# Performance work log

Measured on AMD Instinct MI355X. Metric: run time of the kernel, lower is better.

The kernel has to match this reference:

```python
import jax, jax.numpy as jnp
import numpy as np


def _layernorm(x, g, b, eps=1e-5):
    mu = jnp.mean(x, axis=-1, keepdims=True)
    var = jnp.mean(jnp.square(x - mu), axis=-1, keepdims=True)
    return (x - mu) * jax.lax.rsqrt(var + eps) * g + b


def setup_inputs() -> dict:
    key = jax.random.key(0)
    ks = jax.random.split(key, 8)
    dim, ctx_dim, heads, dim_head = 256, 256, 8, 64
    inner = heads * dim_head
    s = 0.02
    return {
        "x": jax.random.normal(ks[0], (4, dim, 64, 64), jnp.float32),
        "y": jax.random.normal(ks[1], (4, 1024, ctx_dim), jnp.float32),
        "ln_x_g": jnp.ones((dim,), jnp.float32),
        "ln_x_b": jnp.zeros((dim,), jnp.float32),
        "ln_y_g": jnp.ones((ctx_dim,), jnp.float32),
        "ln_y_b": jnp.zeros((ctx_dim,), jnp.float32),
        "Wq": jax.random.normal(ks[2], (dim, inner), jnp.float32) * s,
        "Wk": jax.random.normal(ks[3], (ctx_dim, inner), jnp.float32) * s,
        "Wv": jax.random.normal(ks[4], (ctx_dim, inner), jnp.float32) * s,
        "bv": jnp.zeros((inner,), jnp.float32),
        "Wo": jax.random.normal(ks[5], (inner, dim), jnp.float32) * s,
        "bo": jnp.zeros((dim,), jnp.float32),
    }


def reference(x, y, ln_x_g, ln_x_b, ln_y_g, ln_y_b, Wq, Wk, Wv, bv, Wo, bo):
    heads, dim_head = 8, 64
    b, c = x.shape[:2]
    # channel_last=False path: [b, c, H, W] -> [b, n, c]
    xn = x.reshape(b, c, -1).swapaxes(1, 2)
    xn = _layernorm(xn, ln_x_g, ln_x_b)          # note: x is reassigned in torch code
    yn = _layernorm(y, ln_y_g, ln_y_b)
    q = xn @ Wq                                   # [b, n, h*d]
    k = yn @ Wk                                   # [b, m, h*d]
    v = yn @ Wv + bv                              # [b, m, h*d]

    def split_heads(t):
        B, N, _ = t.shape
        return t.reshape(B, N, heads, dim_head).transpose(0, 2, 1, 3)  # [b, h, n, d]

    q, k, v = split_heads(q), split_heads(k), split_heads(v)
    attn = jnp.einsum("bhid,bhjd->bhij", q, k) * (dim_head ** -0.5)
    attn = jax.nn.softmax(attn, axis=-1)
    out = jnp.einsum("bhij,bhjd->bhid", attn, v)  # [b, h, n, d]
    out = out.transpose(0, 2, 1, 3).reshape(b, -1, heads * dim_head)
    out = out @ Wo + bo
    return xn + out  # residual with layernormed x (faithful to source)
```

## Files before the change

### kernel.cpp

```cpp
#include <hip/hip_runtime.h>
#include <hip/hip_bf16.h>
#include <cstddef>

#define BATCH 4
#define CDIM 256
#define HW 4096
#define MCTX 1024
#define CTX 256
#define HEADS 8
#define DHEAD 64
#define INNER 512

typedef __attribute__((ext_vector_type(8))) short bf16x8;
typedef __attribute__((ext_vector_type(4))) float f32x4;

static __device__ __forceinline__ ushort f2bf(float f) {
  __hip_bfloat16 h = __float2bfloat16(f);
  return *reinterpret_cast<ushort*>(&h);
}

__global__ __launch_bounds__(256) void ln_x_kernel(
    const float* __restrict__ x, const float* __restrict__ g,
    const float* __restrict__ bta, float* __restrict__ xn,
    ushort* __restrict__ xnbf) {
  const int blk = blockIdx.x;
  const int bi = blk / (HW / 32);
  const int n0 = (blk % (HW / 32)) * 32;
  __shared__ float xt[32][257];
  __shared__ float smu[32], srs[32];
  const int t = threadIdx.x;
  const int nl = t & 31;
  const int c0 = t >> 5;
  const float* xb = x + (size_t)bi * CDIM * HW;
  #pragma unroll
  for (int c = c0; c < CDIM; c += 8)
    xt[nl][c] = xb[(size_t)c * HW + n0 + nl];
  __syncthreads();
  const int col = t >> 3, j = t & 7;
  float s = 0.f, ss = 0.f;
  #pragma unroll
  for (int c = j; c < CDIM; c += 8) {
    float v = xt[col][c];
    s += v; ss += v * v;
  }
  #pragma unroll
  for (int off = 1; off < 8; off <<= 1) {
    s += __shfl_xor(s, off);
    ss += __shfl_xor(ss, off);
  }
  if (j == 0) {
    float mu = s * (1.f / CDIM);
    smu[col] = mu;
    srs[col] = rsqrtf(ss * (1.f / CDIM) - mu * mu + 1e-5f);
  }
  __syncthreads();
  const float gv = g[t], bvv = bta[t];
  float* xnb = xn + ((size_t)bi * HW + n0) * CDIM;
  ushort* xbb = xnbf + ((size_t)bi * HW + n0) * CDIM;
  #pragma unroll 4
  for (int n = 0; n < 32; ++n) {
    float val = (xt[n][t] - smu[n]) * srs[n] * gv + bvv;
    xnb[(size_t)n * CDIM + t] = val;
    xbb[(size_t)n * CDIM + t] = f2bf(val);
  }
}

__global__ __launch_bounds__(64) void ln_y_kernel(
    const float* __restrict__ y, const float* __restrict__ g,
    const float* __restrict__ bta, ushort* __restrict__ ynbf) {
  const int row = blockIdx.x;
  const int t = threadIdx.x;
  float4 v = ((const float4*)(y + (size_t)row * CTX))[t];
  float s = v.x + v.y + v.z + v.w;
  float ss = v.x * v.x + v.y * v.y + v.z * v.z + v.w * v.w;
  #pragma unroll
  for (int off = 1; off < 64; off <<= 1) {
    s += __shfl_xor(s, off);
    ss += __shfl_xor(ss, off);
  }
  float mu = s * (1.f / CTX);
  float rs = rsqrtf(ss * (1.f / CTX) - mu * mu + 1e-5f);
  float4 gv = ((const float4*)g)[t];
  float4 b4 = ((const float4*)bta)[t];
  ushort4 ob;
  ob.x = f2bf((v.x - mu) * rs * gv.x + b4.x);
  ob.y = f2bf((v.y - mu) * rs * gv.y + b4.y);
  ob.z = f2bf((v.z - mu) * rs * gv.z + b4.z);
  ob.w = f2bf((v.w - mu) * rs * gv.w + b4.w);
  *(ushort4*)(ynbf + (size_t)row * CTX + t * 4) = ob;
}

__global__ __launch_bounds__(256) void wprep_kernel(
    const float* __restrict__ W, ushort* __restrict__ Wt, int K, int N) {
  __shared__ ushort T[64][65];
  const int k0 = blockIdx.y * 64, n0 = blockIdx.x * 64;
  const int t = threadIdx.x;
  #pragma unroll
  for (int rr = 0; rr < 4; ++rr) {
    int row = rr * 16 + (t >> 4);
    int c = (t & 15) * 4;
    float4 wv = *(const float4*)(W + (size_t)(k0 + row) * N + n0 + c);
    T[row][c + 0] = f2bf(wv.x); T[row][c + 1] = f2bf(wv.y);
    T[row][c + 2] = f2bf(wv.z); T[row][c + 3] = f2bf(wv.w);
  }
  __syncthreads();
  #pragma unroll
  for (int rr = 0; rr < 4; ++rr) {
    int nrow = rr * 16 + (t >> 4);
    int kc = (t & 15) * 4;
    ushort4 o;
    o.x = T[kc + 0][nrow]; o.y = T[kc + 1][nrow];
    o.z = T[kc + 2][nrow]; o.w = T[kc + 3][nrow];
    *(ushort4*)(Wt + (size_t)(n0 + nrow) * K + k0 + kc) = o;
  }
}

__global__ __launch_bounds__(256) void vtr_kernel(
    const ushort* __restrict__ v, ushort* __restrict__ vt) {
  const int bh = blockIdx.z, bi = bh >> 3, h = bh & 7;
  const int m0 = blockIdx.x * 64;
  __shared__ ushort T[64][65];
  const int t = threadIdx.x;
  #pragma unroll
  for (int rr = 0; rr < 4; ++rr) {
    int row = rr * 16 + (t >> 4);
    int c = (t & 15) * 4;
    ushort4 vv = *(const ushort4*)(v + (size_t)(bi * MCTX + m0 + row) * INNER + h * DHEAD + c);
    T[row][c + 0] = vv.x; T[row][c + 1] = vv.y;
    T[row][c + 2] = vv.z; T[row][c + 3] = vv.w;
  }
  __syncthreads();
  #pragma unroll
  for (int rr = 0; rr < 4; ++rr) {
    int drow = rr * 16 + (t >> 4);
    int mc = (t & 15) * 4;
    ushort4 o;
    o.x = T[mc + 0][drow]; o.y = T[mc + 1][drow];
    o.z = T[mc + 2][drow]; o.w = T[mc + 3][drow];
    *(ushort4*)(vt + (size_t)(bh * 64 + drow) * MCTX + m0 + mc) = o;
  }
}

template <bool HAS_BIAS, bool F32_RES_OUT>
__global__ __launch_bounds__(256) void mfma_gemm(
    const ushort* __restrict__ A, const ushort* __restrict__ Bt,
    const float* __restrict__ bias, const float* __restrict__ res,
    void* __restrict__ Cout, int M, int N, int K, float scale) {
  __shared__ ushort As[128 * 40];
  __shared__ ushort Bs[128 * 40];
  const int t = threadIdx.x;
  const int l = t & 63, w = t >> 6;
  const int lq = l & 15, lg = l >> 4;
  const int wr = w >> 1, wc = w & 1;
  const int m0 = blockIdx.y * 128, n0 = blockIdx.x * 128;
  f32x4 acc[4][4];
  #pragma unroll
  for (int mt = 0; mt < 4; ++mt)
    #pragma unroll
    for (int nt = 0; nt < 4; ++nt)
      #pragma unroll
      for (int e = 0; e < 4; ++e) acc[mt][nt][e] = 0.f;
  const int r = t >> 2, ch = (t & 3) * 8;
  for (int k0 = 0; k0 < K; k0 += 32) {
    uint4 a0 = *(const uint4*)(A + (size_t)(m0 + r) * K + k0 + ch);
    uint4 a1 = *(const uint4*)(A + (size_t)(m0 + r + 64) * K + k0 + ch);
    uint4 b0 = *(const uint4*)(Bt + (size_t)(n0 + r) * K + k0 + ch);
    uint4 b1 = *(const uint4*)(Bt + (size_t)(n0 + r + 64) * K + k0 + ch);
    __syncthreads();
    *(uint4*)(&As[r * 40 + ch]) = a0;
    *(uint4*)(&As[(r + 64) * 40 + ch]) = a1;
    *(uint4*)(&Bs[r * 40 + ch]) = b0;
    *(uint4*)(&Bs[(r + 64) * 40 + ch]) = b1;
    __syncthreads();
    bf16x8 af[4], bfr[4];
    #pragma unroll
    for (int mt = 0; mt < 4; ++mt)
      af[mt] = *(const bf16x8*)(&As[(wr * 64 + mt * 16 + lq) * 40 + lg * 8]);
    #pragma unroll
    for (int nt = 0; nt < 4; ++nt)
      bfr[nt] = *(const bf16x8*)(&Bs[(wc * 64 + nt * 16 + lq) * 40 + lg * 8]);
    #pragma unroll
    for (int mt = 0; mt < 4; ++mt)
      #pragma unroll
      for (int nt = 0; nt < 4; ++nt)
        acc[mt][nt] = __builtin_amdgcn_mfma_f32_16x16x32_bf16(
            af[mt], bfr[nt], acc[mt][nt], 0, 0, 0);
  }
  #pragma unroll
  for (int nt = 0; nt < 4; ++nt) {
    const int colc = n0 + wc * 64 + nt * 16 + lq;
    const float bcol = HAS_BIAS ? bias[colc] : 0.f;
    #pragma unroll
    for (int mt = 0; mt < 4; ++mt) {
      #pragma unroll
      for (int i = 0; i < 4; ++i) {
        const size_t row = (size_t)(m0 + wr * 64 + mt * 16 + lg * 4 + i);
        float v = acc[mt][nt][i] * scale + bcol;
        if (F32_RES_OUT) {
          ((float*)Cout)[row * N + colc] = v + res[row * N + colc];
        } else {
          ((ushort*)Cout)[row * N + colc] = f2bf(v);
        }
      }
    }
  }
}

__global__ __launch_bounds__(512, 4) void attn_mfma(
    const ushort* __restrict__ q, const ushort* __restrict__ k,
    const ushort* __restrict__ vt, ushort* __restrict__ ao) {
  const int bi = blockIdx.z, h = blockIdx.y;
  const int n0 = blockIdx.x * 256;
  __shared__ ushort Ks[2][64 * 64];
  __shared__ ushort Vs[2][64 * 64];
  __shared__ ushort Ps[8][2][16 * 64];
  const int t = threadIdx.x;
  const int l = t & 63, w = t >> 6;
  const int lq = l & 15, lg = l >> 4;

  bf16x8 bq[2][2];
  #pragma unroll
  for (int g = 0; g < 2; ++g) {
    const size_t qrow = (size_t)(bi * HW + n0 + w * 32 + g * 16 + lq);
    #pragma unroll
    for (int ks = 0; ks < 2; ++ks)
      bq[g][ks] = *(const bf16x8*)(q + qrow * INNER + h * DHEAD + ks * 32 + lg * 8);
  }

  float m_run[2] = {-1e30f, -1e30f}, l_run[2] = {0.f, 0.f};
  f32x4 oacc[2][4];
  #pragma unroll
  for (int g = 0; g < 2; ++g)
    #pragma unroll
    for (int dt = 0; dt < 4; ++dt)
      #pragma unroll
      for (int e = 0; e < 4; ++e) oacc[g][dt][e] = 0.f;

  const int rr = t >> 3, cc = (t & 7) * 8;
  const ushort* kptr = k + (size_t)(bi * MCTX + rr) * INNER + h * DHEAD + cc;
  const ushort* vptr = vt + (size_t)((bi * HEADS + h) * 64 + rr) * MCTX + cc;
  const int sidx = (rr * 64 + cc) ^ ((rr & 7) << 3);

  {
    uint4 k0v = *(const uint4*)(kptr);
    uint4 v0v = *(const uint4*)(vptr);
    *(uint4*)(&Ks[0][sidx]) = k0v;
    *(uint4*)(&Vs[0][sidx]) = v0v;
  }
  __syncthreads();

  #pragma unroll 2
  for (int m0 = 0; m0 < MCTX; m0 += 64) {
    const int buf = (m0 >> 6) & 1;
    const bool more = (m0 + 64) < MCTX;
    uint4 kpre{}, vpre{};
    if (more) {
      kpre = *(const uint4*)(kptr + (size_t)(m0 + 64) * INNER);
      vpre = *(const uint4*)(vptr + (m0 + 64));
    }
    f32x4 sc[2][4];
    #pragma unroll
    for (int g = 0; g < 2; ++g)
      #pragma unroll
      for (int j = 0; j < 4; ++j)
        #pragma unroll
        for (int e = 0; e < 4; ++e) sc[g][j][e] = 0.f;
    __builtin_amdgcn_s_setprio(1);
    #pragma unroll
    for (int j = 0; j < 4; ++j) {
      #pragma unroll
      for (int ks = 0; ks < 2; ++ks) {
        const int krow = j * 16 + lq;
        bf16x8 ak = *(const bf16x8*)(
            &Ks[buf][(krow * 64 + ks * 32 + lg * 8) ^ ((krow & 7) << 3)]);
        sc[0][j] = __builtin_amdgcn_mfma_f32_16x16x32_bf16(ak, bq[0][ks], sc[0][j], 0, 0, 0);
        sc[1][j] = __builtin_amdgcn_mfma_f32_16x16x32_bf16(ak, bq[1][ks], sc[1][j], 0, 0, 0);
      }
    }
    __builtin_amdgcn_s_setprio(0);
    bf16x8 pa[2][2];
    #pragma unroll
    for (int g = 0; g < 2; ++g) {
      float mloc = -1e30f;
      #pragma unroll
      for (int j = 0; j < 4; ++j)
        #pragma unroll
        for (int e = 0; e < 4; ++e) mloc = fmaxf(mloc, sc[g][j][e]);
      mloc = fmaxf(mloc, __shfl_xor(mloc, 16));
      mloc = fmaxf(mloc, __shfl_xor(mloc, 32));
      if (!__all((int)(mloc - m_run[g] <= 8.f))) {
        const float mnew = fmaxf(m_run[g], mloc);
        const float corr = __builtin_amdgcn_exp2f(m_run[g] - mnew);
        l_run[g] *= corr;
        m_run[g] = mnew;
        #pragma unroll
        for (int i = 0; i < 4; ++i) {
          float ci = __shfl(corr, lg * 4 + i);
          #pragma unroll
          for (int dt = 0; dt < 4; ++dt) oacc[g][dt][i] *= ci;
        }
      }
      float psum = 0.f;
      #pragma unroll
      for (int j = 0; j < 4; ++j)
        #pragma unroll
        for (int e = 0; e < 4; ++e) {
          float p = __builtin_amdgcn_exp2f(sc[g][j][e] - m_run[g]);
          sc[g][j][e] = p; psum += p;
        }
      psum += __shfl_xor(psum, 16);
      psum += __shfl_xor(psum, 32);
      l_run[g] += psum;
      #pragma unroll
      for (int j = 0; j < 4; ++j) {
        uint2 pk;
        pk.x = (uint)f2bf(sc[g][j][0]) | ((uint)f2bf(sc[g][j][1]) << 16);
        pk.y = (uint)f2bf(sc[g][j][2]) | ((uint)f2bf(sc[g][j][3]) << 16);
        *(uint2*)(&Ps[w][g][(lq * 64 + j * 16 + lg * 4) ^ ((lq & 7) << 3)]) = pk;
      }
      #pragma unroll
      for (int ks = 0; ks < 2; ++ks)
        pa[g][ks] = *(const bf16x8*)(
            &Ps[w][g][(lq * 64 + ks * 32 + lg * 8) ^ ((lq & 7) << 3)]);
    }
    __builtin_amdgcn_s_setprio(1);
    #pragma unroll
    for (int dt = 0; dt < 4; ++dt) {
      #pragma unroll
      for (int ks = 0; ks < 2; ++ks) {
        const int vrow = dt * 16 + lq;
        bf16x8 vb = *(const bf16x8*)(
            &Vs[buf][(vrow * 64 + ks * 32 + lg * 8) ^ ((vrow & 7) << 3)]);
        oacc[0][dt] = __builtin_amdgcn_mfma_f32_16x16x32_bf16(pa[0][ks], vb, oacc[0][dt], 0, 0, 0);
        oacc[1][dt] = __builtin_amdgcn_mfma_f32_16x16x32_bf16(pa[1][ks], vb, oacc[1][dt], 0, 0, 0);
      }
    }
    __builtin_amdgcn_s_setprio(0);
    if (more) {
      *(uint4*)(&Ks[buf ^ 1][sidx]) = kpre;
      *(uint4*)(&Vs[buf ^ 1][sidx]) = vpre;
    }
    __syncthreads();
  }
  #pragma unroll
  for (int g = 0; g < 2; ++g) {
    const float rl = 1.f / l_run[g];
    #pragma unroll
    for (int i = 0; i < 4; ++i) {
      float li = __shfl(rl, lg * 4 + i);
      const size_t row = (size_t)(bi * HW + n0 + w * 32 + g * 16 + lg * 4 + i);
      #pragma unroll
      for (int dt = 0; dt < 4; ++dt)
        ao[row * INNER + h * DHEAD + dt * 16 + lq] = f2bf(oacc[g][dt][i] * li);
    }
  }
}

extern "C" void kernel_launch(void* const* d_in, const int* in_sizes, int n_in,
                              void* d_out, int out_size, void* d_ws, size_t ws_size,
                              hipStream_t stream) {
  const float* x     = (const float*)d_in[0];
  const float* y     = (const float*)d_in[1];
  const float* ln_xg = (const float*)d_in[2];
  const float* ln_xb = (const float*)d_in[3];
  const float* ln_yg = (const float*)d_in[4];
  const float* ln_yb = (const float*)d_in[5];
  const float* Wq    = (const float*)d_in[6];
  const float* Wk    = (const float*)d_in[7];
  const float* Wv    = (const float*)d_in[8];
  const float* bv    = (const float*)d_in[9];
  const float* Wo    = (const float*)d_in[10];
  const float* bo    = (const float*)d_in[11];
  float* out = (float*)d_out;

  char* p = (char*)d_ws;
  float*  xn   = (float*)p;  p += (size_t)16384 * 256 * 4;
  ushort* xnbf = (ushort*)p; p += (size_t)16384 * 256 * 2;
  ushort* ynbf = (ushort*)p; p += (size_t)4096 * 256 * 2;
  ushort* wtq  = (ushort*)p; p += (size_t)512 * 256 * 2;
  ushort* wtk  = (ushort*)p; p += (size_t)512 * 256 * 2;
  ushort* wtv  = (ushort*)p; p += (size_t)512 * 256 * 2;
  ushort* wto  = (ushort*)p; p += (size_t)256 * 512 * 2;
  ushort* qbf  = (ushort*)p; p += (size_t)16384 * 512 * 2;
  ushort* kbf  = (ushort*)p; p += (size_t)4096 * 512 * 2;
  ushort* vbf  = (ushort*)p; p += (size_t)4096 * 512 * 2;
  ushort* vtb  = (ushort*)p; p += (size_t)4096 * 512 * 2;
  ushort* aobf = (ushort*)p; p += (size_t)16384 * 512 * 2;

  wprep_kernel<<<dim3(8, 4), 256, 0, stream>>>(Wq, wtq, 256, 512);
  wprep_kernel<<<dim3(8, 4), 256, 0, stream>>>(Wk, wtk, 256, 512);
  wprep_kernel<<<dim3(8, 4), 256, 0, stream>>>(Wv, wtv, 256, 512);
  wprep_kernel<<<dim3(4, 8), 256, 0, stream>>>(Wo, wto, 512, 256);
  ln_x_kernel<<<dim3(BATCH * (HW / 32)), 256, 0, stream>>>(x, ln_xg, ln_xb, xn, xnbf);
  ln_y_kernel<<<dim3(BATCH * MCTX), 64, 0, stream>>>(y, ln_yg, ln_yb, ynbf);
  mfma_gemm<false, false><<<dim3(4, 128), 256, 0, stream>>>(
      xnbf, wtq, nullptr, nullptr, qbf, 16384, 512, 256, 0.1803368801111204f);
  mfma_gemm<false, false><<<dim3(4, 32), 256, 0, stream>>>(
      ynbf, wtk, nullptr, nullptr, kbf, 4096, 512, 256, 1.f);
  mfma_gemm<true, false><<<dim3(4, 32), 256, 0, stream>>>(
      ynbf, wtv, bv, nullptr, vbf, 4096, 512, 256, 1.f);
  vtr_kernel<<<dim3(16, 1, 32), 256, 0, stream>>>(vbf, vtb);
  attn_mfma<<<dim3(HW / 256, HEADS, BATCH), 512, 0, stream>>>(qbf, kbf, vtb, aobf);
  mfma_gemm<true, true><<<dim3(2, 128), 256, 0, stream>>>(
      aobf, wto, bo, xn, out, 16384, 256, 512, 1.f);
}
```

Baseline: 129.8 us.

## Shrink attention blocks, single-buffer K/V, batch weight prep and LN-y rows

The attention kernel moves from 512-thread blocks covering 256 query rows to 256-thread blocks covering 128 rows. It drops LDS double buffering and the two-group P staging to cut shared memory per block and raise occupancy (launch bounds 256,6). In exchange, each K/V tile now needs two barriers, one before and one after the LDS store, and the loop unroll hint is removed. Separately, the three QKV weight-prep launches are merged into one z-indexed launch, and the LN-y kernel processes four rows per 256-thread block to cut launch and block overhead.

New measurement: 381.4 us. 194% more time.

```diff
diff --git a/kernel.cpp b/kernel.cpp
--- a/kernel.cpp
+++ b/kernel.cpp
@@ -65,11 +65,11 @@
   }
 }
 
-__global__ __launch_bounds__(64) void ln_y_kernel(
+__global__ __launch_bounds__(256) void ln_y_kernel(
     const float* __restrict__ y, const float* __restrict__ g,
     const float* __restrict__ bta, ushort* __restrict__ ynbf) {
-  const int row = blockIdx.x;
-  const int t = threadIdx.x;
+  const int row = blockIdx.x * 4 + (threadIdx.x >> 6);
+  const int t = threadIdx.x & 63;
   float4 v = ((const float4*)(y + (size_t)row * CTX))[t];
   float s = v.x + v.y + v.z + v.w;
   float ss = v.x * v.x + v.y * v.y + v.z * v.z + v.w * v.w;
@@ -90,7 +90,7 @@
   *(ushort4*)(ynbf + (size_t)row * CTX + t * 4) = ob;
 }
 
-__global__ __launch_bounds__(256) void wprep_kernel(
+static __device__ __forceinline__ void wprep_body(
     const float* __restrict__ W, ushort* __restrict__ Wt, int K, int N) {
   __shared__ ushort T[64][65];
   const int k0 = blockIdx.y * 64, n0 = blockIdx.x * 64;
@@ -113,6 +113,21 @@
     o.z = T[kc + 2][nrow]; o.w = T[kc + 3][nrow];
     *(ushort4*)(Wt + (size_t)(n0 + nrow) * K + k0 + kc) = o;
   }
+}
+
+__global__ __launch_bounds__(256) void wprep3_kernel(
+    const float* __restrict__ W0, const float* __restrict__ W1,
+    const float* __restrict__ W2, ushort* __restrict__ T0,
+    ushort* __restrict__ T1, ushort* __restrict__ T2) {
+  const int z = blockIdx.z;
+  const float* W = (z == 0) ? W0 : (z == 1) ? W1 : W2;
+  ushort* Wt = (z == 0) ? T0 : (z == 1) ? T1 : T2;
+  wprep_body(W, Wt, 256, 512);
+}
+
+__global__ __launch_bounds__(256) void wprep_kernel(
+    const float* __restrict__ W, ushort* __restrict__ Wt, int K, int N) {
+  wprep_body(W, Wt, K, N);
 }
 
 __global__ __launch_bounds__(256) void vtr_kernel(
@@ -206,14 +221,14 @@
   }
 }
 
-__global__ __launch_bounds__(512, 4) void attn_mfma(
+__global__ __launch_bounds__(256, 6) void attn_mfma(
     const ushort* __restrict__ q, const ushort* __restrict__ k,
     const ushort* __restrict__ vt, ushort* __restrict__ ao) {
   const int bi = blockIdx.z, h = blockIdx.y;
-  const int n0 = blockIdx.x * 256;
-  __shared__ ushort Ks[2][64 * 64];
-  __shared__ ushort Vs[2][64 * 64];
-  __shared__ ushort Ps[8][2][16 * 64];
+  const int n0 = blockIdx.x * 128;
+  __shared__ ushort Ks[64 * 64];
+  __shared__ ushort Vs[64 * 64];
+  __shared__ ushort Ps[4][16 * 64];
   const int t = threadIdx.x;
   const int l = t & 63, w = t >> 6;
   const int lq = l & 15, lg = l >> 4;
@@ -236,27 +251,32 @@
       #pragma unroll
       for (int e = 0; e < 4; ++e) oacc[g][dt][e] = 0.f;
 
-  const int rr = t >> 3, cc = (t & 7) * 8;
-  const ushort* kptr = k + (size_t)(bi * MCTX + rr) * INNER + h * DHEAD + cc;
-  const ushort* vptr = vt + (size_t)((bi * HEADS + h) * 64 + rr) * MCTX + cc;
-  const int sidx = (rr * 64 + cc) ^ ((rr & 7) << 3);
+  const int rr0 = t >> 3, cc0 = (t & 7) * 8;
+  const int rr1 = (t + 256) >> 3, cc1 = cc0;
+  const ushort* kbase = k + (size_t)bi * MCTX * INNER + h * DHEAD;
+  const ushort* vbase = vt + (size_t)((bi * HEADS + h) * 64) * MCTX;
+  const int sidx0 = (rr0 * 64 + cc0) ^ ((rr0 & 7) << 3);
+  const int sidx1 = (rr1 * 64 + cc1) ^ ((rr1 & 7) << 3);
 
   {
-    uint4 k0v = *(const uint4*)(kptr);
-    uint4 v0v = *(const uint4*)(vptr);
-    *(uint4*)(&Ks[0][sidx]) = k0v;
-    *(uint4*)(&Vs[0][sidx]) = v0v;
+    uint4 ka = *(const uint4*)(kbase + (size_t)rr0 * INNER + cc0);
+    uint4 kb2 = *(const uint4*)(kbase + (size_t)rr1 * INNER + cc1);
+    uint4 va = *(const uint4*)(vbase + (size_t)rr0 * MCTX + cc0);
+    uint4 vb2 = *(const uint4*)(vbase + (size_t)rr1 * MCTX + cc1);
+    *(uint4*)(&Ks[sidx0]) = ka;  *(uint4*)(&Ks[sidx1]) = kb2;
+    *(uint4*)(&Vs[sidx0]) = va;  *(uint4*)(&Vs[sidx1]) = vb2;
   }
   __syncthreads();
 
-  #pragma unroll 2
   for (int m0 = 0; m0 < MCTX; m0 += 64) {
-    const int buf = (m0 >> 6) & 1;
     const bool more = (m0 + 64) < MCTX;
-    uint4 kpre{}, vpre{};
+    uint4 kp0{}, kp1{}, vp0{}, vp1{};
     if (more) {
-      kpre = *(const uint4*)(kptr + (size_t)(m0 + 64) * INNER);
-      vpre = *(const uint4*)(vptr + (m0 + 64));
+      const int mn = m0 + 64;
+      kp0 = *(const uint4*)(kbase + (size_t)(mn + rr0) * INNER + cc0);
+      kp1 = *(const uint4*)(kbase + (size_t)(mn + rr1) * INNER + cc1);
+      vp0 = *(const uint4*)(vbase + (size_t)rr0 * MCTX + mn + cc0);
+      vp1 = *(const uint4*)(vbase + (size_t)rr1 * MCTX + mn + cc1);
     }
     f32x4 sc[2][4];
     #pragma unroll
@@ -272,7 +292,7 @@
       for (int ks = 0; ks < 2; ++ks) {
         const int krow = j * 16 + lq;
         bf16x8 ak = *(const bf16x8*)(
-            &Ks[buf][(krow * 64 + ks * 32 + lg * 8) ^ ((krow & 7) << 3)]);
+            &Ks[(krow * 64 + ks * 32 + lg * 8) ^ ((krow & 7) << 3)]);
         sc[0][j] = __builtin_amdgcn_mfma_f32_16x16x32_bf16(ak, bq[0][ks], sc[0][j], 0, 0, 0);
         sc[1][j] = __builtin_amdgcn_mfma_f32_16x16x32_bf16(ak, bq[1][ks], sc[1][j], 0, 0, 0);
       }
@@ -316,12 +336,12 @@
         uint2 pk;
         pk.x = (uint)f2bf(sc[g][j][0]) | ((uint)f2bf(sc[g][j][1]) << 16);
         pk.y = (uint)f2bf(sc[g][j][2]) | ((uint)f2bf(sc[g][j][3]) << 16);
-        *(uint2*)(&Ps[w][g][(lq * 64 + j * 16 + lg * 4) ^ ((lq & 7) << 3)]) = pk;
+        *(uint2*)(&Ps[w][(lq * 64 + j * 16 + lg * 4) ^ ((lq & 7) << 3)]) = pk;
       }
       #pragma unroll
       for (int ks = 0; ks < 2; ++ks)
         pa[g][ks] = *(const bf16x8*)(
-            &Ps[w][g][(lq * 64 + ks * 32 + lg * 8) ^ ((lq & 7) << 3)]);
+            &Ps[w][(lq * 64 + ks * 32 + lg * 8) ^ ((lq & 7) << 3)]);
     }
     __builtin_amdgcn_s_setprio(1);
     #pragma unroll
@@ -330,17 +350,18 @@
       for (int ks = 0; ks < 2; ++ks) {
         const int vrow = dt * 16 + lq;
         bf16x8 vb = *(const bf16x8*)(
-            &Vs[buf][(vrow * 64 + ks * 32 + lg * 8) ^ ((vrow & 7) << 3)]);
+            &Vs[(vrow * 64 + ks * 32 + lg * 8) ^ ((vrow & 7) << 3)]);
         oacc[0][dt] = __builtin_amdgcn_mfma_f32_16x16x32_bf16(pa[0][ks], vb, oacc[0][dt], 0, 0, 0);
         oacc[1][dt] = __builtin_amdgcn_mfma_f32_16x16x32_bf16(pa[1][ks], vb, oacc[1][dt], 0, 0, 0);
       }
     }
     __builtin_amdgcn_s_setprio(0);
     if (more) {
-      *(uint4*)(&Ks[buf ^ 1][sidx]) = kpre;
-      *(uint4*)(&Vs[buf ^ 1][sidx]) = vpre;
-    }
-    __syncthreads();
+      __syncthreads();
+      *(uint4*)(&Ks[sidx0]) = kp0;  *(uint4*)(&Ks[sidx1]) = kp1;
+      *(uint4*)(&Vs[sidx0]) = vp0;  *(uint4*)(&Vs[sidx1]) = vp1;
+      __syncthreads();
+    }
   }
   #pragma unroll
   for (int g = 0; g < 2; ++g) {
@@ -387,12 +408,10 @@
   ushort* vtb  = (ushort*)p; p += (size_t)4096 * 512 * 2;
   ushort* aobf = (ushort*)p; p += (size_t)16384 * 512 * 2;
 
-  wprep_kernel<<<dim3(8, 4), 256, 0, stream>>>(Wq, wtq, 256, 512);
-  wprep_kernel<<<dim3(8, 4), 256, 0, stream>>>(Wk, wtk, 256, 512);
-  wprep_kernel<<<dim3(8, 4), 256, 0, stream>>>(Wv, wtv, 256, 512);
+  wprep3_kernel<<<dim3(8, 4, 3), 256, 0, stream>>>(Wq, Wk, Wv, wtq, wtk, wtv);
   wprep_kernel<<<dim3(4, 8), 256, 0, stream>>>(Wo, wto, 512, 256);
   ln_x_kernel<<<dim3(BATCH * (HW / 32)), 256, 0, stream>>>(x, ln_xg, ln_xb, xn, xnbf);
-  ln_y_kernel<<<dim3(BATCH * MCTX), 64, 0, stream>>>(y, ln_yg, ln_yb, ynbf);
+  ln_y_kernel<<<dim3(BATCH * MCTX / 4), 256, 0, stream>>>(y, ln_yg, ln_yb, ynbf);
   mfma_gemm<false, false><<<dim3(4, 128), 256, 0, stream>>>(
       xnbf, wtq, nullptr, nullptr, qbf, 16384, 512, 256, 0.1803368801111204f);
   mfma_gemm<false, false><<<dim3(4, 32), 256, 0, stream>>>(
@@ -400,7 +419,7 @@
   mfma_gemm<true, false><<<dim3(4, 32), 256, 0, stream>>>(
       ynbf, wtv, bv, nullptr, vbf, 4096, 512, 256, 1.f);
   vtr_kernel<<<dim3(16, 1, 32), 256, 0, stream>>>(vbf, vtb);
-  attn_mfma<<<dim3(HW / 256, HEADS, BATCH), 512, 0, stream>>>(qbf, kbf, vtb, aobf);
+  attn_mfma<<<dim3(HW / 128, HEADS, BATCH), 256, 0, stream>>>(qbf, kbf, vtb, aobf);
   mfma_gemm<true, true><<<dim3(2, 128), 256, 0, stream>>>(
       aobf, wto, bo, xn, out, 16384, 256, 512, 1.f);
 }
```

## Merge weight-prep launches, pack ln_y rows, swizzle attention blocks, move prefetch stores

Applied to the files above, without the earlier changes.

Merges the three QKV weight-conversion launches into one 3D-grid kernel and packs four ln_y rows into each 256-thread block, cutting launch count and tiny-block overhead. The attention kernel remaps block IDs so consecutive blocks land on different (batch, head) groups, which changes L2 and XCD locality for K/V reuse. Its softmax is moved into a lambda, and the next-tile K/V shared-memory stores now sit between the two row-group softmaxes instead of after the PV MFMAs, to hide their latency behind ALU work. The block swizzle may hurt cache locality if heads sharing K/V end up on different XCDs.

Result: faster. 124.7 us (-3.9%).

```diff
diff --git a/kernel.cpp b/kernel.cpp
--- a/kernel.cpp
+++ b/kernel.cpp
@@ -65,11 +65,11 @@
   }
 }
 
-__global__ __launch_bounds__(64) void ln_y_kernel(
+__global__ __launch_bounds__(256) void ln_y_kernel(
     const float* __restrict__ y, const float* __restrict__ g,
     const float* __restrict__ bta, ushort* __restrict__ ynbf) {
-  const int row = blockIdx.x;
-  const int t = threadIdx.x;
+  const int row = blockIdx.x * 4 + (threadIdx.x >> 6);
+  const int t = threadIdx.x & 63;
   float4 v = ((const float4*)(y + (size_t)row * CTX))[t];
   float s = v.x + v.y + v.z + v.w;
   float ss = v.x * v.x + v.y * v.y + v.z * v.z + v.w * v.w;
@@ -90,7 +90,7 @@
   *(ushort4*)(ynbf + (size_t)row * CTX + t * 4) = ob;
 }
 
-__global__ __launch_bounds__(256) void wprep_kernel(
+static __device__ __forceinline__ void wprep_body(
     const float* __restrict__ W, ushort* __restrict__ Wt, int K, int N) {
   __shared__ ushort T[64][65];
   const int k0 = blockIdx.y * 64, n0 = blockIdx.x * 64;
@@ -113,6 +113,21 @@
     o.z = T[kc + 2][nrow]; o.w = T[kc + 3][nrow];
     *(ushort4*)(Wt + (size_t)(n0 + nrow) * K + k0 + kc) = o;
   }
+}
+
+__global__ __launch_bounds__(256) void wprep3_kernel(
+    const float* __restrict__ W0, const float* __restrict__ W1,
+    const float* __restrict__ W2, ushort* __restrict__ T0,
+    ushort* __restrict__ T1, ushort* __restrict__ T2) {
+  const int z = blockIdx.z;
+  const float* W = (z == 0) ? W0 : (z == 1) ? W1 : W2;
+  ushort* Wt = (z == 0) ? T0 : (z == 1) ? T1 : T2;
+  wprep_body(W, Wt, 256, 512);
+}
+
+__global__ __launch_bounds__(256) void wprep_kernel(
+    const float* __restrict__ W, ushort* __restrict__ Wt, int K, int N) {
+  wprep_body(W, Wt, K, N);
 }
 
 __global__ __launch_bounds__(256) void vtr_kernel(
@@ -209,8 +224,11 @@
 __global__ __launch_bounds__(512, 4) void attn_mfma(
     const ushort* __restrict__ q, const ushort* __restrict__ k,
     const ushort* __restrict__ vt, ushort* __restrict__ ao) {
-  const int bi = blockIdx.z, h = blockIdx.y;
-  const int n0 = blockIdx.x * 256;
+  const int bid = blockIdx.x + 16 * (blockIdx.y + 8 * blockIdx.z);
+  const int swz = (bid & 7) * 64 + (bid >> 3);
+  const int bi = swz >> 7;
+  const int h = (swz >> 4) & 7;
+  const int n0 = (swz & 15) * 256;
   __shared__ ushort Ks[2][64 * 64];
   __shared__ ushort Vs[2][64 * 64];
   __shared__ ushort Ps[8][2][16 * 64];
@@ -248,6 +266,47 @@
     *(uint4*)(&Vs[0][sidx]) = v0v;
   }
   __syncthreads();
+
+  auto softmax_group = [&](f32x4 (&scg)[4], float& mr, float& lr,
+                           f32x4 (&oa)[4], ushort* psw) {
+    float mloc = -1e30f;
+    #pragma unroll
+    for (int j = 0; j < 4; ++j)
+      #pragma unroll
+      for (int e = 0; e < 4; ++e) mloc = fmaxf(mloc, scg[j][e]);
+    mloc = fmaxf(mloc, __shfl_xor(mloc, 16));
+    mloc = fmaxf(mloc, __shfl_xor(mloc, 32));
+    if (!__all((int)(mloc - mr <= 8.f))) {
+      const float mnew = fmaxf(mr, mloc);
+      const float corr = __builtin_amdgcn_exp2f(mr - mnew);
+      lr *= corr;
+      mr = mnew;
+      #pragma unroll
+      for (int i = 0; i < 4; ++i) {
+        float ci = __shfl(corr, lg * 4 + i);
+        #pragma unroll
+        for (int dt = 0; dt < 4; ++dt) oa[dt][i] *= ci;
+      }
+    }
+    float psum = 0.f;
+    #pragma unroll
+    for (int j = 0; j < 4; ++j)
+      #pragma unroll
+      for (int e = 0; e < 4; ++e) {
+        float p = __builtin_amdgcn_exp2f(scg[j][e] - mr);
+        scg[j][e] = p; psum += p;
+      }
+    psum += __shfl_xor(psum, 16);
+    psum += __shfl_xor(psum, 32);
+    lr += psum;
+    #pragma unroll
+    for (int j = 0; j < 4; ++j) {
+      uint2 pk;
+      pk.x = (uint)f2bf(scg[j][0]) | ((uint)f2bf(scg[j][1]) << 16);
+      pk.y = (uint)f2bf(scg[j][2]) | ((uint)f2bf(scg[j][3]) << 16);
+      *(uint2*)(psw + ((lq * 64 + j * 16 + lg * 4) ^ ((lq & 7) << 3))) = pk;
+    }
+  };
 
   #pragma unroll 2
   for (int m0 = 0; m0 < MCTX; m0 += 64) {
@@ -278,51 +337,19 @@
       }
     }
     __builtin_amdgcn_s_setprio(0);
+    softmax_group(sc[0], m_run[0], l_run[0], oacc[0], &Ps[w][0][0]);
+    if (more) {
+      *(uint4*)(&Ks[buf ^ 1][sidx]) = kpre;
+      *(uint4*)(&Vs[buf ^ 1][sidx]) = vpre;
+    }
+    softmax_group(sc[1], m_run[1], l_run[1], oacc[1], &Ps[w][1][0]);
     bf16x8 pa[2][2];
     #pragma unroll
-    for (int g = 0; g < 2; ++g) {
-      float mloc = -1e30f;
-      #pragma unroll
-      for (int j = 0; j < 4; ++j)
-        #pragma unroll
-        for (int e = 0; e < 4; ++e) mloc = fmaxf(mloc, sc[g][j][e]);
-      mloc = fmaxf(mloc, __shfl_xor(mloc, 16));
-      mloc = fmaxf(mloc, __shfl_xor(mloc, 32));
-      if (!__all((int)(mloc - m_run[g] <= 8.f))) {
-        const float mnew = fmaxf(m_run[g], mloc);
-        const float corr = __builtin_amdgcn_exp2f(m_run[g] - mnew);
-        l_run[g] *= corr;
-        m_run[g] = mnew;
-        #pragma unroll
-        for (int i = 0; i < 4; ++i) {
-          float ci = __shfl(corr, lg * 4 + i);
-          #pragma unroll
-          for (int dt = 0; dt < 4; ++dt) oacc[g][dt][i] *= ci;
-        }
-      }
-      float psum = 0.f;
-      #pragma unroll
-      for (int j = 0; j < 4; ++j)
-        #pragma unroll
-        for (int e = 0; e < 4; ++e) {
-          float p = __builtin_amdgcn_exp2f(sc[g][j][e] - m_run[g]);
-          sc[g][j][e] = p; psum += p;
-        }
-      psum += __shfl_xor(psum, 16);
-      psum += __shfl_xor(psum, 32);
-      l_run[g] += psum;
-      #pragma unroll
-      for (int j = 0; j < 4; ++j) {
-        uint2 pk;
-        pk.x = (uint)f2bf(sc[g][j][0]) | ((uint)f2bf(sc[g][j][1]) << 16);
-        pk.y = (uint)f2bf(sc[g][j][2]) | ((uint)f2bf(sc[g][j][3]) << 16);
-        *(uint2*)(&Ps[w][g][(lq * 64 + j * 16 + lg * 4) ^ ((lq & 7) << 3)]) = pk;
-      }
+    for (int g = 0; g < 2; ++g)
       #pragma unroll
       for (int ks = 0; ks < 2; ++ks)
         pa[g][ks] = *(const bf16x8*)(
             &Ps[w][g][(lq * 64 + ks * 32 + lg * 8) ^ ((lq & 7) << 3)]);
-    }
     __builtin_amdgcn_s_setprio(1);
     #pragma unroll
     for (int dt = 0; dt < 4; ++dt) {
@@ -336,10 +363,6 @@
       }
     }
     __builtin_amdgcn_s_setprio(0);
-    if (more) {
-      *(uint4*)(&Ks[buf ^ 1][sidx]) = kpre;
-      *(uint4*)(&Vs[buf ^ 1][sidx]) = vpre;
-    }
     __syncthreads();
   }
   #pragma unroll
@@ -387,12 +410,10 @@
   ushort* vtb  = (ushort*)p; p += (size_t)4096 * 512 * 2;
   ushort* aobf = (ushort*)p; p += (size_t)16384 * 512 * 2;
 
-  wprep_kernel<<<dim3(8, 4), 256, 0, stream>>>(Wq, wtq, 256, 512);
-  wprep_kernel<<<dim3(8, 4), 256, 0, stream>>>(Wk, wtk, 256, 512);
-  wprep_kernel<<<dim3(8, 4), 256, 0, stream>>>(Wv, wtv, 256, 512);
+  wprep3_kernel<<<dim3(8, 4, 3), 256, 0, stream>>>(Wq, Wk, Wv, wtq, wtk, wtv);
   wprep_kernel<<<dim3(4, 8), 256, 0, stream>>>(Wo, wto, 512, 256);
   ln_x_kernel<<<dim3(BATCH * (HW / 32)), 256, 0, stream>>>(x, ln_xg, ln_xb, xn, xnbf);
-  ln_y_kernel<<<dim3(BATCH * MCTX), 64, 0, stream>>>(y, ln_yg, ln_yb, ynbf);
+  ln_y_kernel<<<dim3(BATCH * MCTX / 4), 256, 0, stream>>>(y, ln_yg, ln_yb, ynbf);
   mfma_gemm<false, false><<<dim3(4, 128), 256, 0, stream>>>(
       xnbf, wtq, nullptr, nullptr, qbf, 16384, 512, 256, 0.1803368801111204f);
   mfma_gemm<false, false><<<dim3(4, 32), 256, 0, stream>>>(
```
